# Optimization experiments

Measured on AMD Instinct MI355X. Metric: run time of the kernel, lower is better.

The kernel has to match this reference:

```python
import jax, jax.numpy as jnp
import numpy as np

N_NEWS = 200000
N_COMPANIES = 10000
N_EDGES = 640000
HIDDEN = 256


def setup_inputs() -> dict:
    key = jax.random.key(0)
    ks = jax.random.split(key, 7)
    scale = 1.0 / np.sqrt(HIDDEN)  # keep tanh out of full saturation
    news_x = jax.random.normal(ks[0], (N_NEWS, HIDDEN), dtype=jnp.float32)
    company_x = jax.random.normal(ks[1], (N_COMPANIES, HIDDEN), dtype=jnp.float32)
    W_news = jax.random.normal(ks[2], (HIDDEN, HIDDEN), dtype=jnp.float32) * scale
    W_company = jax.random.normal(ks[3], (HIDDEN, HIDDEN), dtype=jnp.float32) * scale
    v = jax.random.normal(ks[4], (HIDDEN,), dtype=jnp.float32) * scale
    src = jax.random.randint(ks[5], (N_EDGES,), 0, N_NEWS, dtype=jnp.int64)
    dst = jax.random.randint(ks[6], (N_EDGES,), 0, N_COMPANIES, dtype=jnp.int64)
    return {
        "news_x": news_x,
        "company_x": company_x,
        "W_news": W_news,
        "W_company": W_company,
        "v": v,
        "src": src,
        "dst": dst,
        "num_companies": N_COMPANIES,
    }


def reference(news_x, company_x, W_news, W_company, v, src, dst, num_companies):
    # Gather per-edge endpoint features, project (nn.Linear applies x @ W.T).
    news_part = news_x[src] @ W_news.T          # [E, H]
    company_part = company_x[dst] @ W_company.T  # [E, H]
    scores = jnp.tanh(news_part + company_part) @ v  # [E]

    # Segment-wise (per-company) numerically stable softmax over incoming edges.
    smax = jax.ops.segment_max(scores, dst, num_segments=num_companies)  # [C]
    scores_exp = jnp.exp(scores - smax[dst])                             # [E]
    denom = jax.ops.segment_sum(scores_exp, dst, num_segments=num_companies)[dst]
    weights = scores_exp / jnp.clip(denom, 1e-9)                         # [E]

    # Weighted scatter-add of raw news features into company slots.
    out = jax.ops.segment_sum(news_x[src] * weights[:, None], dst,
                              num_segments=num_companies)               # [C, H]
    return out
```

## Files before the change

### kernel.cpp

```cpp
#include <hip/hip_runtime.h>
#include <hip/hip_bf16.h>
#include <cmath>
#include <cstdint>


#define H 256

typedef __attribute__((ext_vector_type(8))) short bfrag;
typedef __attribute__((ext_vector_type(4))) float ffrag;

__device__ __forceinline__ ushort f2bf(float f) {
  uint u = __float_as_uint(f);
  uint r = u + 0x7FFFu + ((u >> 16) & 1u);
  return (ushort)(r >> 16);
}
__device__ __forceinline__ float bf2f(ushort h) {
  return __uint_as_float((uint)h << 16);
}

__global__ void prep_kernel(const float* __restrict__ Wn, const float* __restrict__ Wc,
                            ushort* __restrict__ WnHi, ushort* __restrict__ WnLo,
                            ushort* __restrict__ WcHi, ushort* __restrict__ WcLo,
                            const int* __restrict__ dst, int* __restrict__ counts, int E) {
  const int b = blockIdx.x, tid = threadIdx.x;
  if (b < 256) {
    int i = b * 256 + tid;
    float w = Wn[i];
    ushort h = f2bf(w);
    WnHi[i] = h;
    WnLo[i] = f2bf(w - bf2f(h));
  } else if (b < 512) {
    int i = (b - 256) * 256 + tid;
    float w = Wc[i];
    ushort h = f2bf(w);
    WcHi[i] = h;
    WcLo[i] = f2bf(w - bf2f(h));
  } else {
    int e = (b - 512) * 256 + tid;
    if (e < E) atomicAdd(&counts[dst[e]], 1);
  }
}

__global__ void scan_kernel(const int* __restrict__ counts, int* __restrict__ offsets,
                            int* __restrict__ cursor, int C) {
  __shared__ int wsum[16];
  int tid = threadIdx.x;
  int lane = tid & 63, wid = tid >> 6;
  int base = 0;
  for (int start = 0; start < C; start += 1024) {
    int idx = start + tid;
    int val = (idx < C) ? counts[idx] : 0;
    int x = val;
#pragma unroll
    for (int off = 1; off < 64; off <<= 1) {
      int y = __shfl_up(x, off);
      if (lane >= off) x += y;
    }
    if (lane == 63) wsum[wid] = x;
    __syncthreads();
    int add = base;
    for (int w = 0; w < wid; ++w) add += wsum[w];
    if (idx < C) {
      int excl = add + x - val;
      offsets[idx] = excl;
      cursor[idx]  = excl;
    }
    int tot = 0;
#pragma unroll
    for (int w = 0; w < 16; ++w) tot += wsum[w];
    __syncthreads();
    base += tot;
  }
  if (tid == 0) offsets[C] = base;
}

__global__ void fill_kernel(const int* __restrict__ src, const int* __restrict__ dst,
                            int* __restrict__ cursor, int* __restrict__ srcs_sorted, int E) {
  int e = blockIdx.x * blockDim.x + threadIdx.x;
  if (e < E) {
    int d = dst[e];
    int pos = atomicAdd(&cursor[d], 1);
    srcs_sorted[pos] = src[e];
  }
}

__global__ __launch_bounds__(512, 2) void gemm_persist(
    const float* __restrict__ Xc, const ushort* __restrict__ WcHi,
    const ushort* __restrict__ WcLo, ushort* __restrict__ cproj, int MC, int GC,
    const float* __restrict__ Xn, const ushort* __restrict__ WnHi,
    const ushort* __restrict__ WnLo, ushort* __restrict__ nproj,
    ushort* __restrict__ nxbf, int MN) {
  constexpr int PITCH = 264;
  __shared__ ushort Xs[2][64 * PITCH];
  const int tid = threadIdx.x;
  const int wv = tid >> 6, lane = tid & 63;
  const int q = lane >> 4, nidx = lane & 15;
  const int GN = gridDim.x - GC;

  const float* X; const ushort *Whi, *Wlo; ushort *proj, *xb; int M, nb, lb;
  if ((int)blockIdx.x < GC) {
    X = Xc; Whi = WcHi; Wlo = WcLo; proj = cproj; xb = nullptr; M = MC;
    nb = GC; lb = blockIdx.x;
  } else {
    X = Xn; Whi = WnHi; Wlo = WnLo; proj = nproj; xb = nxbf; M = MN;
    nb = GN; lb = blockIdx.x - GC;
  }
  const int nt = (M + 63) >> 6;
  const int qt = nt / nb, rt = nt % nb;
  const int first = lb * qt + (lb < rt ? lb : rt);
  const int cnt = qt + (lb < rt ? 1 : 0);
  if (cnt <= 0) return;

  bfrag bhi[8][2], blo[8][2];
#pragma unroll
  for (int ks = 0; ks < 8; ++ks)
#pragma unroll
    for (int tt = 0; tt < 2; ++tt) {
      const size_t off = (size_t)(wv * 32 + tt * 16 + nidx) * H + ks * 32 + q * 8;
      bhi[ks][tt] = *(const bfrag*)(Whi + off);
      blo[ks][tt] = *(const bfrag*)(Wlo + off);
    }

  float4 xr[8];
  auto load8 = [&](int tile) {
#pragma unroll
    for (int j = 0; j < 8; ++j) {
      const int flat = j * 2048 + tid * 4;
      int gr = tile * 64 + (flat >> 8);
      if (gr >= M) gr = M - 1;
      xr[j] = *(const float4*)(X + (size_t)gr * H + (flat & 255));
    }
  };
  auto writebuf = [&](int p, int tile) {
#pragma unroll
    for (int j = 0; j < 8; ++j) {
      const int flat = j * 2048 + tid * 4;
      const int r = flat >> 8, k = flat & 255;
      ushort4 b4;
      b4.x = f2bf(xr[j].x); b4.y = f2bf(xr[j].y);
      b4.z = f2bf(xr[j].z); b4.w = f2bf(xr[j].w);
      *(ushort4*)&Xs[p][r * PITCH + k] = b4;
      if (xb) {
        const int gr = tile * 64 + r;
        *(ushort4*)(xb + (size_t)gr * H + k) = b4;
      }
    }
  };

  load8(first);
  writebuf(0, first);
  int p = 0;
  for (int t = 0; t < cnt; ++t) {
    __syncthreads();
    const int tile = first + t;
    const bool more = (t + 1 < cnt);
    if (more) load8(tile + 1);

    ffrag acc[4][2];
#pragma unroll
    for (int i = 0; i < 4; ++i) { acc[i][0] = (ffrag)(0.f); acc[i][1] = (ffrag)(0.f); }
#pragma unroll
    for (int ks = 0; ks < 8; ++ks) {
      bfrag a[4];
#pragma unroll
      for (int i = 0; i < 4; ++i)
        a[i] = *(const bfrag*)&Xs[p][(16 * i + nidx) * PITCH + ks * 32 + q * 8];
#pragma unroll
      for (int i = 0; i < 4; ++i)
#pragma unroll
        for (int tt = 0; tt < 2; ++tt) {
          acc[i][tt] = __builtin_amdgcn_mfma_f32_16x16x32_bf16(a[i], bhi[ks][tt], acc[i][tt], 0, 0, 0);
          acc[i][tt] = __builtin_amdgcn_mfma_f32_16x16x32_bf16(a[i], blo[ks][tt], acc[i][tt], 0, 0, 0);
        }
    }

    const int row0 = tile * 64;
#pragma unroll
    for (int i = 0; i < 4; ++i)
#pragma unroll
      for (int r = 0; r < 4; ++r) {
        const int grow = row0 + 16 * i + q * 4 + r;
        if (grow < M) {
#pragma unroll
          for (int tt = 0; tt < 2; ++tt)
            proj[(size_t)grow * H + wv * 32 + tt * 16 + nidx] = f2bf(acc[i][tt][r]);
        }
      }

    if (more) writebuf(p ^ 1, tile + 1);
    p ^= 1;
  }
}

__device__ __forceinline__ float fast_tanh(float x) {
  float e = __expf(2.f * x);
  return 1.f - 2.f / (e + 1.f);
}

__device__ __forceinline__ float score_dot(ushort4 p, float4 cq, float4 vv) {
  float r = fast_tanh(bf2f(p.x) + cq.x) * vv.x + fast_tanh(bf2f(p.y) + cq.y) * vv.y +
            fast_tanh(bf2f(p.z) + cq.z) * vv.z + fast_tanh(bf2f(p.w) + cq.w) * vv.w;
#pragma unroll
  for (int off = 32; off > 0; off >>= 1) r += __shfl_xor(r, off);
  return r;
}

__global__ __launch_bounds__(256) void edge_flash_kernel(
    const ushort* __restrict__ news_projbf, const ushort* __restrict__ company_projbf,
    const float* __restrict__ v, const int* __restrict__ offsets,
    const int* __restrict__ srcs, const ushort* __restrict__ news_xbf,
    float* __restrict__ out) {
  const int c = blockIdx.x;
  const int tid = threadIdx.x, lane = tid & 63, wid = tid >> 6;
  __shared__ float cp[H];
  __shared__ float mW[4], lW[4];
  __shared__ float OW[4][H];
  cp[tid] = bf2f(company_projbf[(size_t)c * H + tid]);
  __syncthreads();
  const float4 vv = *(const float4*)(v + lane * 4);
  const float4 cq = *(const float4*)&cp[lane * 4];
  const int beg = offsets[c], end = offsets[c + 1];

  float m = -INFINITY, l = 0.f;
  float4 O = make_float4(0.f, 0.f, 0.f, 0.f);

  int i = beg + wid * 2;
  if (i + 1 < end) {
    int s0 = srcs[i], s1 = srcs[i + 1];
    ushort4 p0 = *(const ushort4*)(news_projbf + (size_t)s0 * H + lane * 4);
    ushort4 p1 = *(const ushort4*)(news_projbf + (size_t)s1 * H + lane * 4);
    ushort4 x0 = *(const ushort4*)(news_xbf + (size_t)s0 * H + lane * 4);
    ushort4 x1 = *(const ushort4*)(news_xbf + (size_t)s1 * H + lane * 4);
    for (;;) {
      const int inext = i + 8;
      const bool more = (inext + 1 < end);
      ushort4 np0, np1, nx0, nx1;
      if (more) {
        int t0 = srcs[inext], t1 = srcs[inext + 1];
        np0 = *(const ushort4*)(news_projbf + (size_t)t0 * H + lane * 4);
        np1 = *(const ushort4*)(news_projbf + (size_t)t1 * H + lane * 4);
        nx0 = *(const ushort4*)(news_xbf + (size_t)t0 * H + lane * 4);
        nx1 = *(const ushort4*)(news_xbf + (size_t)t1 * H + lane * 4);
      }
      const float sa = score_dot(p0, cq, vv);
      const float sb = score_dot(p1, cq, vv);
      const float mnew = fmaxf(m, fmaxf(sa, sb));
      const float alpha = __expf(m - mnew);
      const float pa = __expf(sa - mnew);
      const float pb = __expf(sb - mnew);
      l = l * alpha + pa + pb;
      O.x = O.x * alpha + pa * bf2f(x0.x) + pb * bf2f(x1.x);
      O.y = O.y * alpha + pa * bf2f(x0.y) + pb * bf2f(x1.y);
      O.z = O.z * alpha + pa * bf2f(x0.z) + pb * bf2f(x1.z);
      O.w = O.w * alpha + pa * bf2f(x0.w) + pb * bf2f(x1.w);
      m = mnew;
      i = inext;
      if (!more) break;
      p0 = np0; p1 = np1; x0 = nx0; x1 = nx1;
    }
  }
  if (i < end) {
    const int s0 = srcs[i];
    const ushort4 p0 = *(const ushort4*)(news_projbf + (size_t)s0 * H + lane * 4);
    const ushort4 x0 = *(const ushort4*)(news_xbf + (size_t)s0 * H + lane * 4);
    const float sa = score_dot(p0, cq, vv);
    const float mnew = fmaxf(m, sa);
    const float alpha = __expf(m - mnew);
    const float pa = __expf(sa - mnew);
    l = l * alpha + pa;
    O.x = O.x * alpha + pa * bf2f(x0.x);
    O.y = O.y * alpha + pa * bf2f(x0.y);
    O.z = O.z * alpha + pa * bf2f(x0.z);
    O.w = O.w * alpha + pa * bf2f(x0.w);
    m = mnew;
  }

  if (lane == 0) { mW[wid] = m; lW[wid] = l; }
  *(float4*)&OW[wid][lane * 4] = O;
  __syncthreads();
  const float mstar = fmaxf(fmaxf(mW[0], mW[1]), fmaxf(mW[2], mW[3]));
  float denom = 0.f, val = 0.f;
#pragma unroll
  for (int w = 0; w < 4; ++w) {
    const float sc = (lW[w] > 0.f) ? __expf(mW[w] - mstar) : 0.f;
    denom += lW[w] * sc;
    val += OW[w][tid] * sc;
  }
  out[(size_t)c * H + tid] = val / fmaxf(denom, 1e-9f);
}

extern "C" void kernel_launch(void* const* d_in, const int* in_sizes, int n_in,
                              void* d_out, int out_size, void* d_ws, size_t ws_size,
                              hipStream_t stream) {
  const float* news_x    = (const float*)d_in[0];
  const float* company_x = (const float*)d_in[1];
  const float* W_news    = (const float*)d_in[2];
  const float* W_company = (const float*)d_in[3];
  const float* v         = (const float*)d_in[4];
  const int*   src       = (const int*)d_in[5];
  const int*   dst       = (const int*)d_in[6];
  const int N = in_sizes[0] / H;
  const int C = in_sizes[1] / H;
  const int E = in_sizes[5];
  float* out = (float*)d_out;

  char* p = (char*)d_ws;
  ushort* news_projbf    = (ushort*)p; p += (size_t)N * H * sizeof(ushort);
  ushort* news_xbf       = (ushort*)p; p += (size_t)N * H * sizeof(ushort);
  ushort* company_projbf = (ushort*)p; p += (size_t)C * H * sizeof(ushort);
  int*    srcs_sorted    = (int*)p;    p += (size_t)E * sizeof(int);
  ushort* Wn_hi          = (ushort*)p; p += (size_t)H * H * sizeof(ushort);
  ushort* Wn_lo          = (ushort*)p; p += (size_t)H * H * sizeof(ushort);
  ushort* Wc_hi          = (ushort*)p; p += (size_t)H * H * sizeof(ushort);
  ushort* Wc_lo          = (ushort*)p; p += (size_t)H * H * sizeof(ushort);
  int*    counts         = (int*)p;    p += (size_t)C * sizeof(int);
  int*    offsets        = (int*)p;    p += (size_t)(C + 1) * sizeof(int);
  int*    cursor         = (int*)p;    p += (size_t)C * sizeof(int);

  hipMemsetAsync(counts, 0, (size_t)C * sizeof(int), stream);
  prep_kernel<<<512 + (E + 255) / 256, 256, 0, stream>>>(
      W_news, W_company, Wn_hi, Wn_lo, Wc_hi, Wc_lo, dst, counts, E);
  scan_kernel<<<1, 1024, 0, stream>>>(counts, offsets, cursor, C);
  fill_kernel<<<(E + 255) / 256, 256, 0, stream>>>(src, dst, cursor, srcs_sorted, E);

  const int GC = 24, GN = 488;
  gemm_persist<<<GC + GN, 512, 0, stream>>>(
      company_x, Wc_hi, Wc_lo, company_projbf, C, GC,
      news_x, Wn_hi, Wn_lo, news_projbf, news_xbf, N);

  edge_flash_kernel<<<C, 256, 0, stream>>>(news_projbf, company_projbf, v, offsets,
                                           srcs_sorted, news_xbf, out);
}
```

Measured before the change: 556.1 us.

## Process one edge per half-wave with 8-wide bf16 loads and cheaper tanh

The edge softmax-aggregation kernel now assigns one edge per 32-lane half-wave, with each lane covering 8 hidden elements through 16-byte loads, in place of two edges per 64-lane wave with 8-byte loads. This shortens the shuffle reduction from 6 to 5 steps and lets 8 independent streams merge in the final reduction. tanh now uses hardware exp2 and rcp intrinsics instead of expf plus a true division. In exchange it uses more registers per lane and adds a larger shared-memory merge across 8 partial states.

```diff
diff --git a/kernel.cpp b/kernel.cpp
--- a/kernel.cpp
+++ b/kernel.cpp
@@ -193,16 +193,9 @@
 }
 
 __device__ __forceinline__ float fast_tanh(float x) {
-  float e = __expf(2.f * x);
-  return 1.f - 2.f / (e + 1.f);
-}
-
-__device__ __forceinline__ float score_dot(ushort4 p, float4 cq, float4 vv) {
-  float r = fast_tanh(bf2f(p.x) + cq.x) * vv.x + fast_tanh(bf2f(p.y) + cq.y) * vv.y +
-            fast_tanh(bf2f(p.z) + cq.z) * vv.z + fast_tanh(bf2f(p.w) + cq.w) * vv.w;
-#pragma unroll
-  for (int off = 32; off > 0; off >>= 1) r += __shfl_xor(r, off);
-  return r;
+  float e = __builtin_amdgcn_exp2f(x * 2.8853900817779268f);
+  float t = __builtin_amdgcn_rcpf(e + 1.f);
+  return __builtin_fmaf(-2.f, t, 1.f);
 }
 
 __global__ __launch_bounds__(256) void edge_flash_kernel(
@@ -211,77 +204,71 @@
     const int* __restrict__ srcs, const ushort* __restrict__ news_xbf,
     float* __restrict__ out) {
   const int c = blockIdx.x;
-  const int tid = threadIdx.x, lane = tid & 63, wid = tid >> 6;
+  const int tid = threadIdx.x;
+  const int sl = tid & 31;
+  const int hw = tid >> 5;
   __shared__ float cp[H];
-  __shared__ float mW[4], lW[4];
-  __shared__ float OW[4][H];
+  __shared__ float mW[8], lW[8];
+  __shared__ float OW[8][H];
   cp[tid] = bf2f(company_projbf[(size_t)c * H + tid]);
   __syncthreads();
-  const float4 vv = *(const float4*)(v + lane * 4);
-  const float4 cq = *(const float4*)&cp[lane * 4];
+  const float4 va = *(const float4*)(v + sl * 8);
+  const float4 vb = *(const float4*)(v + sl * 8 + 4);
+  const float4 ca = *(const float4*)&cp[sl * 8];
+  const float4 cb = *(const float4*)&cp[sl * 8 + 4];
+  const float vv[8] = {va.x, va.y, va.z, va.w, vb.x, vb.y, vb.z, vb.w};
+  const float cq[8] = {ca.x, ca.y, ca.z, ca.w, cb.x, cb.y, cb.z, cb.w};
   const int beg = offsets[c], end = offsets[c + 1];
 
   float m = -INFINITY, l = 0.f;
-  float4 O = make_float4(0.f, 0.f, 0.f, 0.f);
-
-  int i = beg + wid * 2;
-  if (i + 1 < end) {
-    int s0 = srcs[i], s1 = srcs[i + 1];
-    ushort4 p0 = *(const ushort4*)(news_projbf + (size_t)s0 * H + lane * 4);
-    ushort4 p1 = *(const ushort4*)(news_projbf + (size_t)s1 * H + lane * 4);
-    ushort4 x0 = *(const ushort4*)(news_xbf + (size_t)s0 * H + lane * 4);
-    ushort4 x1 = *(const ushort4*)(news_xbf + (size_t)s1 * H + lane * 4);
+  float O[8] = {0.f, 0.f, 0.f, 0.f, 0.f, 0.f, 0.f, 0.f};
+
+  int i = beg + hw;
+  if (i < end) {
+    int s = srcs[i];
+    bfrag pr = *(const bfrag*)(news_projbf + (size_t)s * H + sl * 8);
+    bfrag xr = *(const bfrag*)(news_xbf + (size_t)s * H + sl * 8);
     for (;;) {
       const int inext = i + 8;
-      const bool more = (inext + 1 < end);
-      ushort4 np0, np1, nx0, nx1;
+      const bool more = (inext < end);
+      bfrag prn, xrn;
       if (more) {
-        int t0 = srcs[inext], t1 = srcs[inext + 1];
-        np0 = *(const ushort4*)(news_projbf + (size_t)t0 * H + lane * 4);
-        np1 = *(const ushort4*)(news_projbf + (size_t)t1 * H + lane * 4);
-        nx0 = *(const ushort4*)(news_xbf + (size_t)t0 * H + lane * 4);
-        nx1 = *(const ushort4*)(news_xbf + (size_t)t1 * H + lane * 4);
+        int sn = srcs[inext];
+        prn = *(const bfrag*)(news_projbf + (size_t)sn * H + sl * 8);
+        xrn = *(const bfrag*)(news_xbf + (size_t)sn * H + sl * 8);
       }
-      const float sa = score_dot(p0, cq, vv);
-      const float sb = score_dot(p1, cq, vv);
-      const float mnew = fmaxf(m, fmaxf(sa, sb));
+      float r = 0.f;
+#pragma unroll
+      for (int j = 0; j < 8; ++j)
+        r += fast_tanh(bf2f((ushort)pr[j]) + cq[j]) * vv[j];
+#pragma unroll
+      for (int off = 16; off > 0; off >>= 1) r += __shfl_xor(r, off);
+      const float mnew = fmaxf(m, r);
       const float alpha = __expf(m - mnew);
-      const float pa = __expf(sa - mnew);
-      const float pb = __expf(sb - mnew);
-      l = l * alpha + pa + pb;
-      O.x = O.x * alpha + pa * bf2f(x0.x) + pb * bf2f(x1.x);
-      O.y = O.y * alpha + pa * bf2f(x0.y) + pb * bf2f(x1.y);
-      O.z = O.z * alpha + pa * bf2f(x0.z) + pb * bf2f(x1.z);
-      O.w = O.w * alpha + pa * bf2f(x0.w) + pb * bf2f(x1.w);
+      const float pa = __expf(r - mnew);
+      l = l * alpha + pa;
+#pragma unroll
+      for (int j = 0; j < 8; ++j)
+        O[j] = O[j] * alpha + pa * bf2f((ushort)xr[j]);
       m = mnew;
       i = inext;
       if (!more) break;
-      p0 = np0; p1 = np1; x0 = nx0; x1 = nx1;
-    }
-  }
-  if (i < end) {
-    const int s0 = srcs[i];
-    const ushort4 p0 = *(const ushort4*)(news_projbf + (size_t)s0 * H + lane * 4);
-    const ushort4 x0 = *(const ushort4*)(news_xbf + (size_t)s0 * H + lane * 4);
-    const float sa = score_dot(p0, cq, vv);
-    const float mnew = fmaxf(m, sa);
-    const float alpha = __expf(m - mnew);
-    const float pa = __expf(sa - mnew);
-    l = l * alpha + pa;
-    O.x = O.x * alpha + pa * bf2f(x0.x);
-    O.y = O.y * alpha + pa * bf2f(x0.y);
-    O.z = O.z * alpha + pa * bf2f(x0.z);
-    O.w = O.w * alpha + pa * bf2f(x0.w);
-    m = mnew;
-  }
-
-  if (lane == 0) { mW[wid] = m; lW[wid] = l; }
-  *(float4*)&OW[wid][lane * 4] = O;
+      pr = prn; xr = xrn;
+    }
+  }
+
+  if (sl == 0) { mW[hw] = m; lW[hw] = l; }
+  float4 oa = make_float4(O[0], O[1], O[2], O[3]);
+  float4 ob = make_float4(O[4], O[5], O[6], O[7]);
+  *(float4*)&OW[hw][sl * 8] = oa;
+  *(float4*)&OW[hw][sl * 8 + 4] = ob;
   __syncthreads();
-  const float mstar = fmaxf(fmaxf(mW[0], mW[1]), fmaxf(mW[2], mW[3]));
+  float mstar = -INFINITY;
+#pragma unroll
+  for (int w = 0; w < 8; ++w) mstar = fmaxf(mstar, mW[w]);
   float denom = 0.f, val = 0.f;
 #pragma unroll
-  for (int w = 0; w < 4; ++w) {
+  for (int w = 0; w < 8; ++w) {
     const float sc = (lW[w] > 0.f) ? __expf(mW[w] - mstar) : 0.f;
     denom += lW[w] * sc;
     val += OW[w][tid] * sc;
```

Measured after the change: 534.3 us. 1.04x faster.
